# Optimization experiments

Measured on AMD Instinct MI355X. Metric: run time of the kernel, lower is better.

## Reference

```python
import jax, jax.numpy as jnp
import numpy as np

B, C, L, E = 32, 3, 512, 512


def setup_inputs() -> dict:
    key = jax.random.key(0)
    ks = jax.random.split(key, 13)
    bnd = float(np.sqrt(6.0 / (2.0 * E)))  # xavier-uniform-like bound
    uni = lambda k, shp: jax.random.uniform(k, shp, jnp.float32, -bnd, bnd)
    return {
        "A0": jax.random.normal(ks[0], (B, C, L, L), jnp.float32),
        "x0": jax.random.normal(ks[1], (B, C, L, E), jnp.float32),
        "u0": jax.random.normal(ks[2], (B, C, E), jnp.float32),
        "t0": jax.random.normal(ks[3], (B, E), jnp.float32),
        "t1": jax.random.normal(ks[4], (B, E), jnp.float32),
        "Q_weight": uni(ks[5], (C, E, E)),
        "Q_bias": jnp.zeros((C, E), jnp.float32),
        "V_weight": uni(ks[6], (C, E, E)),
        "V_bias": jnp.zeros((C, E), jnp.float32),
        "K_weight": uni(ks[7], (C, E, E)),
        "K_bias": jnp.zeros((C, E), jnp.float32),
        "T_weight": uni(ks[8], (C, E, E)),
        "T_bias": jnp.zeros((C, E), jnp.float32),
    }


def reference(A0, x0, u0, t0, t1,
              Q_weight, Q_bias, V_weight, V_bias,
              K_weight, K_bias, T_weight, T_bias):
    # Time embeddings: (B,E) @ (C,E,E) -> (B,C,E)
    T0 = jnp.einsum('be,cef->bcf', t0, T_weight)
    T1 = jnp.einsum('be,cef->bcf', t1, T_weight)

    # Original modulates weight columns: x @ (W * T) == (x @ W) * T (T broadcasts
    # over the input axis via unsqueeze(-2)); use the fused, equivalent form.
    Q = jnp.einsum('bce,cef->bcf', x0[:, :, -1, :], Q_weight) * T0 + Q_bias  # (B,C,E)
    K = jnp.einsum('bce,cef->bcf', u0, K_weight) * T1 + K_bias               # (B,C,E)
    V = jnp.einsum('bcle,cef->bclf', x0, V_weight) * T1[:, :, None, :] \
        + V_bias[None, :, None, :]                                           # (B,C,L,E)

    QKV = jax.nn.softmax(jnp.einsum('bce,bcle->bcl', Q * K, V), axis=-1)     # (B,C,L)

    # A1[:, :, i, :] = A0[:, :, i+1, :] - A0[:, :, 0, :] for i < L-1;
    # A1[:, :, L-1, :] = A1[:, :, L-2, :] + QKV  (= A0[-1] - A0[0] + QKV)
    rows = A0[:, :, 1:, :] - A0[:, :, :1, :]                                 # (B,C,L-1,L)
    last = rows[:, :, -1, :] + QKV                                           # (B,C,L)
    A1 = jnp.concatenate([rows, last[:, :, None, :]], axis=2)                # (B,C,L,L)

    x1 = jnp.einsum('bclm,bcme->bcle', A1, x0)                               # (B,C,L,E)
    x1 = jnp.diff(x1, axis=2, prepend=jnp.zeros_like(x1[:, :, :1, :]))

    num = jnp.sum(T0 * T1, axis=-1)                                          # (B,C)
    den = jnp.sqrt(jnp.sum(T0 * T0, axis=-1) + jnp.sum(T1 * T1, axis=-1))
    w = (num / den)[..., None]                                               # (B,C,1)

    u1 = u0 * (1.0 - w) + x1.mean(axis=-2) * w                               # (B,C,E)
    return (A1 - A0, x1 - x0, u1 - u0)
```

## Files before the change

kernel.cpp:

```cpp
#include <hip/hip_runtime.h>
#include <stdint.h>

#define BB 32
#define CC 3
#define LL 512
#define EE 512
#define NBC (BB*CC)

#define O2_OFF ((size_t)NBC*LL*LL)
#define O3_OFF (O2_OFF + (size_t)NBC*LL*EE)

#define WSB_QX    0
#define WSB_H     196608
#define WSB_W     442368
#define WSB_ADIFF ((size_t)512*1024)
#define ADIFF_BYTES ((size_t)NBC*LL*LL*2)
#define WSB_X0T   (WSB_ADIFF + ADIFF_BYTES)
#define WS_FAST_NEED (WSB_X0T + ADIFF_BYTES)

#define NEC 16

typedef short bf16x8 __attribute__((ext_vector_type(8)));
typedef float f32x4  __attribute__((ext_vector_type(4)));
typedef unsigned short u16x8 __attribute__((ext_vector_type(8)));

__device__ __forceinline__ float wred_sum(float v){
#pragma unroll
  for (int m = 32; m >= 1; m >>= 1) v += __shfl_xor(v, m, 64);
  return v;
}
__device__ __forceinline__ float wred_max(float v){
#pragma unroll
  for (int m = 32; m >= 1; m >>= 1) v = fmaxf(v, __shfl_xor(v, m, 64));
  return v;
}
__device__ __forceinline__ void f4ma(float4& a, float s, const float4& b){
  a.x = fmaf(s, b.x, a.x); a.y = fmaf(s, b.y, a.y);
  a.z = fmaf(s, b.z, a.z); a.w = fmaf(s, b.w, a.w);
}
__device__ __forceinline__ float4 f4sub(const float4& a, const float4& b){
  return make_float4(a.x-b.x, a.y-b.y, a.z-b.z, a.w-b.w);
}
__device__ __forceinline__ unsigned short f2bf(float x){
  unsigned u = __float_as_uint(x);
  return (unsigned short)((u + 0x7FFFu + ((u >> 16) & 1u)) >> 16);
}
__device__ __forceinline__ float bf2f(unsigned short h){
  return __uint_as_float(((unsigned)h) << 16);
}
__device__ __forceinline__ void split1(float v, unsigned short& hi, unsigned short& lo){
  hi = f2bf(v);
  lo = f2bf(v - bf2f(hi));
}
__device__ __forceinline__ void st_nt_f4(float* p, float4 v){
  f32x4 w; w[0]=v.x; w[1]=v.y; w[2]=v.z; w[3]=v.w;
  __builtin_nontemporal_store(w, reinterpret_cast<f32x4*>(p));
}
__device__ __forceinline__ void st_nt_f(float* p, float v){
  __builtin_nontemporal_store(v, p);
}

__global__ __launch_bounds__(512) void conv2m(
    const float* __restrict__ A0, const float* __restrict__ x0,
    const float* __restrict__ u0,
    const float* __restrict__ t0, const float* __restrict__ t1,
    const float* __restrict__ Qw, const float* __restrict__ Kw,
    const float* __restrict__ Tw,
    char* __restrict__ adiff, char* __restrict__ x0t,
    float* __restrict__ P)
{
  const int bid = blockIdx.x;
  const int t = threadIdx.x;
  __shared__ float T[64][65];
  __shared__ float vb[4][4][32];

  if (bid < 768) {
    const int bc = bid >> 3, tile = bid & 7;
    const int r0 = tile*64;
    const size_t abase = (size_t)bc*LL*LL;
    char* ad = adiff + (size_t)bc*LL*LL*2;
    const int q4 = t & 127, rg = t >> 7;
    const int base = r0 + rg*16;
    float4 prev = *reinterpret_cast<const float4*>(A0 + abase + (size_t)base*LL + q4*4);
#pragma unroll 4
    for (int i = 0; i < 16; ++i) {
      int gr = base + i;
      float4 cur;
      if (gr + 1 < LL)
        cur = *reinterpret_cast<const float4*>(A0 + abase + (size_t)(gr+1)*LL + q4*4);
      else cur = prev;
      float4 d;
      if (gr < LL-1) d = f4sub(cur, prev);
      else           d = make_float4(0.f,0.f,0.f,0.f);
      if ((gr >> 2) == q4) {
        int e = gr & 3;
        d.x -= (e == 0) ? 1.0f : 0.0f;
        d.y -= (e == 1) ? 1.0f : 0.0f;
        d.z -= (e == 2) ? 1.0f : 0.0f;
        d.w -= (e == 3) ? 1.0f : 0.0f;
      }
      ushort4 pk;
      pk.x = f2bf(d.x); pk.y = f2bf(d.y); pk.z = f2bf(d.z); pk.w = f2bf(d.w);
      *reinterpret_cast<ushort4*>(ad + (size_t)gr*1024 + q4*8) = pk;
      prev = cur;
    }
  } else if (bid < 1536) {
    const int bid1 = bid - 768;
    const int bc = bid1 >> 3, tile = bid1 & 7;
    const int m0 = tile*64;
    const size_t xbase = (size_t)bc*LL*EE;
    char* xt = x0t + (size_t)bc*LL*EE*2;
    u16x8 outs[8];
#pragma unroll
    for (int ech = 0; ech < 8; ++ech) {
      const int e0 = ech*64;
      {
        int ml = t >> 3, seg = t & 7;
        const float* src = x0 + xbase + (size_t)(m0+ml)*EE + e0 + seg*8;
        float4 v0 = *reinterpret_cast<const float4*>(src);
        float4 v1 = *reinterpret_cast<const float4*>(src+4);
        T[ml][seg*8+0]=v0.x; T[ml][seg*8+1]=v0.y; T[ml][seg*8+2]=v0.z; T[ml][seg*8+3]=v0.w;
        T[ml][seg*8+4]=v1.x; T[ml][seg*8+5]=v1.y; T[ml][seg*8+6]=v1.z; T[ml][seg*8+7]=v1.w;
      }
      __syncthreads();
      {
        int el = t >> 3, c3 = t & 7;
        int mb = c3*8;
        u16x8 p;
        p[0]=f2bf(T[mb+0][el]); p[1]=f2bf(T[mb+1][el]);
        p[2]=f2bf(T[mb+2][el]); p[3]=f2bf(T[mb+3][el]);
        p[4]=f2bf(T[mb+4][el]); p[5]=f2bf(T[mb+5][el]);
        p[6]=f2bf(T[mb+6][el]); p[7]=f2bf(T[mb+7][el]);
        outs[ech] = p;
      }
      __syncthreads();
    }
    {
      int el = t >> 3, c3 = t & 7;
#pragma unroll
      for (int ech = 0; ech < 8; ++ech) {
        int eg = ech*64 + el;
        *reinterpret_cast<u16x8*>(xt + (size_t)eg*1024 + (size_t)(m0 + c3*8)*2) = outs[ech];
      }
    }
  } else {
    const int idx = bid - 1536;
    const int bg = idx & 7;
    const int rem = idx >> 3;
    const int c  = rem % 3;
    const int ec = rem / 3;
    const int b0 = bg*4;
    const int e0 = ec*32;
    const int f  = t;
    {
      int vec = f >> 7, j = (f >> 5) & 3, e = f & 31;
      int bb = b0 + j;
      float v;
      if      (vec == 0) v = t0[bb*EE + e0 + e];
      else if (vec == 1) v = t1[bb*EE + e0 + e];
      else if (vec == 2) v = x0[((size_t)(bb*CC + c)*LL + (LL-1))*EE + e0 + e];
      else               v = u0[(size_t)(bb*CC + c)*EE + e0 + e];
      vb[vec][j][e] = v;
    }
    __syncthreads();
    const float* twp = Tw + (size_t)c*EE*EE + (size_t)e0*EE + f;
    const float* qwp = Qw + (size_t)c*EE*EE + (size_t)e0*EE + f;
    const float* kwp = Kw + (size_t)c*EE*EE + (size_t)e0*EE + f;
    float aT0[4]={0,0,0,0}, aT1[4]={0,0,0,0}, aQ[4]={0,0,0,0}, aK[4]={0,0,0,0};
#pragma unroll 8
    for (int e = 0; e < 32; ++e) {
      float wt = twp[(size_t)e*EE];
      float wq = qwp[(size_t)e*EE];
      float wk = kwp[(size_t)e*EE];
#pragma unroll
      for (int j = 0; j < 4; ++j) {
        aT0[j] = fmaf(vb[0][j][e], wt, aT0[j]);
        aT1[j] = fmaf(vb[1][j][e], wt, aT1[j]);
        aQ[j]  = fmaf(vb[2][j][e], wq, aQ[j]);
        aK[j]  = fmaf(vb[3][j][e], wk, aK[j]);
      }
    }
#pragma unroll
    for (int j = 0; j < 4; ++j) {
      int cb = c*BB + b0 + j;
      P[(((size_t)0*NEC + ec)*96 + cb)*EE + f] = aT0[j];
      P[(((size_t)1*NEC + ec)*96 + cb)*EE + f] = aT1[j];
      P[(((size_t)2*NEC + ec)*96 + cb)*EE + f] = aQ[j];
      P[(((size_t)3*NEC + ec)*96 + cb)*EE + f] = aK[j];
    }
  }
}

__global__ __launch_bounds__(512) void k0c(
    const float* __restrict__ P,
    const float* __restrict__ Qb, const float* __restrict__ Kb,
    float* __restrict__ gtbuf, float* __restrict__ ws_w)
{
  const int bc = blockIdx.x;
  const int b = bc / CC, c = bc % CC;
  const int cb = c*BB + b;
  const int f = threadIdx.x;
  const int wid = f >> 6, lane = f & 63;
  __shared__ float red[8][3];
  float aT0=0.f, aT1=0.f, aQ=0.f, aK=0.f;
#pragma unroll
  for (int ec = 0; ec < NEC; ++ec) {
    aT0 += P[(((size_t)0*NEC + ec)*96 + cb)*EE + f];
    aT1 += P[(((size_t)1*NEC + ec)*96 + cb)*EE + f];
    aQ  += P[(((size_t)2*NEC + ec)*96 + cb)*EE + f];
    aK  += P[(((size_t)3*NEC + ec)*96 + cb)*EE + f];
  }
  float Qv = aQ*aT0 + Qb[c*EE + f];
  float Kv = aK*aT1 + Kb[c*EE + f];
  gtbuf[(size_t)cb*EE + f] = Qv*Kv*aT1;
  float pn = wred_sum(aT0*aT1);
  float p0 = wred_sum(aT0*aT0);
  float p1 = wred_sum(aT1*aT1);
  if (lane == 0) { red[wid][0]=pn; red[wid][1]=p0; red[wid][2]=p1; }
  __syncthreads();
  if (f == 0) {
    float sn=0.f, s0=0.f, s1=0.f;
    for (int i=0;i<8;++i){ sn+=red[i][0]; s0+=red[i][1]; s1+=red[i][2]; }
    ws_w[bc] = sn / sqrtf(s0 + s1);
  }
}

__global__ __launch_bounds__(256) void k1_h(
    const float* __restrict__ Vw, const float* __restrict__ gtbuf,
    float* __restrict__ ws_h)
{
  const int nt = blockIdx.x;
  const int c  = blockIdx.y;
  const int n0 = nt*128;
  const int t = threadIdx.x, lane = t & 63, w = t >> 6;
  __shared__ __align__(16) char AgtH[32*1024];
  __shared__ __align__(16) char AgtL[32*1024];
  __shared__ __align__(16) char BvH[128*128];
  __shared__ __align__(16) char BvL[128*128];
  {
    int row = t >> 3, sl = t & 7;
    const float* src = gtbuf + ((size_t)(c*BB + row))*EE + sl*64;
#pragma unroll
    for (int c3 = 0; c3 < 8; ++c3) {
      float4 a = *reinterpret_cast<const float4*>(src + c3*8);
      float4 b = *reinterpret_cast<const float4*>(src + c3*8 + 4);
      ushort4 h0,h1,l0,l1;
      split1(a.x,h0.x,l0.x); split1(a.y,h0.y,l0.y); split1(a.z,h0.z,l0.z); split1(a.w,h0.w,l0.w);
      split1(b.x,h1.x,l1.x); split1(b.y,h1.y,l1.y); split1(b.z,h1.z,l1.z); split1(b.w,h1.w,l1.w);
      int off = row*1024 + sl*128 + ((c3 ^ (row & 7)) << 4);
      *reinterpret_cast<ushort4*>(AgtH + off)     = h0;
      *reinterpret_cast<ushort4*>(AgtH + off + 8) = h1;
      *reinterpret_cast<ushort4*>(AgtL + off)     = l0;
      *reinterpret_cast<ushort4*>(AgtL + off + 8) = l1;
    }
  }
  f32x4 acc[2][2];
#pragma unroll
  for (int mi=0; mi<2; ++mi)
#pragma unroll
    for (int ni=0; ni<2; ++ni) acc[mi][ni] = (f32x4){0.f,0.f,0.f,0.f};

  for (int kk = 0; kk < 8; ++kk) {
    __syncthreads();
    {
      int nl = t >> 1, half = t & 1;
      const float* src = Vw + (size_t)c*EE*EE + (size_t)(n0+nl)*EE + kk*64 + half*32;
#pragma unroll
      for (int q = 0; q < 4; ++q) {
        float4 a = *reinterpret_cast<const float4*>(src + q*8);
        float4 b = *reinterpret_cast<const float4*>(src + q*8 + 4);
        int c3 = half*4 + q;
        ushort4 h0,h1,l0,l1;
        split1(a.x,h0.x,l0.x); split1(a.y,h0.y,l0.y); split1(a.z,h0.z,l0.z); split1(a.w,h0.w,l0.w);
        split1(b.x,h1.x,l1.x); split1(b.y,h1.y,l1.y); split1(b.z,h1.z,l1.z); split1(b.w,h1.w,l1.w);
        int off = nl*128 + ((c3 ^ (nl & 7)) << 4);
        *reinterpret_cast<ushort4*>(BvH + off)     = h0;
        *reinterpret_cast<ushort4*>(BvH + off + 8) = h1;
        *reinterpret_cast<ushort4*>(BvL + off)     = l0;
        *reinterpret_cast<ushort4*>(BvL + off + 8) = l1;
      }
    }
    __syncthreads();
    bf16x8 afH[2][2], afL[2][2], bfH[2][2], bfL[2][2];
#pragma unroll
    for (int mi=0; mi<2; ++mi)
#pragma unroll
      for (int ks=0; ks<2; ++ks) {
        int row = mi*16 + (lane & 15);
        int c3 = ks*4 + (lane >> 4);
        int off = row*1024 + kk*128 + ((c3 ^ (row & 7)) << 4);
        afH[mi][ks] = *reinterpret_cast<const bf16x8*>(AgtH + off);
        afL[mi][ks] = *reinterpret_cast<const bf16x8*>(AgtL + off);
      }
#pragma unroll
    for (int ni=0; ni<2; ++ni)
#pragma unroll
      for (int ks=0; ks<2; ++ks) {
        int n = w*32 + ni*16 + (lane & 15);
        int c3 = ks*4 + (lane >> 4);
        int off = n*128 + ((c3 ^ (n & 7)) << 4);
        bfH[ni][ks] = *reinterpret_cast<const bf16x8*>(BvH + off);
        bfL[ni][ks] = *reinterpret_cast<const bf16x8*>(BvL + off);
      }
#pragma unroll
    for (int mi=0; mi<2; ++mi)
#pragma unroll
      for (int ni=0; ni<2; ++ni)
#pragma unroll
        for (int ks=0; ks<2; ++ks) {
          acc[mi][ni] = __builtin_amdgcn_mfma_f32_16x16x32_bf16(afH[mi][ks], bfH[ni][ks], acc[mi][ni], 0, 0, 0);
          acc[mi][ni] = __builtin_amdgcn_mfma_f32_16x16x32_bf16(afH[mi][ks], bfL[ni][ks], acc[mi][ni], 0, 0, 0);
          acc[mi][ni] = __builtin_amdgcn_mfma_f32_16x16x32_bf16(afL[mi][ks], bfH[ni][ks], acc[mi][ni], 0, 0, 0);
        }
  }
#pragma unroll
  for (int mi=0; mi<2; ++mi)
#pragma unroll
    for (int ni=0; ni<2; ++ni)
#pragma unroll
      for (int r=0; r<4; ++r) {
        int b = mi*16 + (lane >> 4)*4 + r;
        int e = n0 + w*32 + ni*16 + (lane & 15);
        ws_h[((size_t)(b*CC + c))*EE + e] = acc[mi][ni][r];
      }
}

__global__ __launch_bounds__(512) void k2f(
    const float* __restrict__ A0, const float* __restrict__ x0,
    const float* __restrict__ u0,
    const float* __restrict__ ws_h, const float* __restrict__ ws_w,
    float* __restrict__ out1, float* __restrict__ out2, float* __restrict__ out3)
{
  const int bc = blockIdx.x;
  const int tid = threadIdx.x, wid = tid >> 6, lane = tid & 63;
  __shared__ __align__(16) float hb[EE], sb[LL], a0r0[LL], a0r3[LL];
  __shared__ float red[8];
  __shared__ float partl[4][12][128];
  const size_t abase = (size_t)bc*LL*LL;
  const size_t xbase = (size_t)bc*LL*EE;
  hb[tid]   = ws_h[(size_t)bc*EE + tid];
  a0r0[tid] = A0[abase + tid];
  a0r3[tid] = A0[abase + (size_t)(LL-1)*LL + tid];
  __syncthreads();
  const float4 h0 = *reinterpret_cast<const float4*>(&hb[lane*8]);
  const float4 h1 = *reinterpret_cast<const float4*>(&hb[lane*8+4]);
  for (int l = wid; l < LL; l += 8) {
    const float4* xr = reinterpret_cast<const float4*>(x0 + xbase + (size_t)l*EE);
    float4 v0 = xr[lane*2], v1 = xr[lane*2+1];
    float acc = v0.x*h0.x + v0.y*h0.y + v0.z*h0.z + v0.w*h0.w
              + v1.x*h1.x + v1.y*h1.y + v1.z*h1.z + v1.w*h1.w;
    acc = wred_sum(acc);
    if (lane == 0) sb[l] = acc;
  }
  __syncthreads();
  float v = sb[tid];
  float mx = wred_max(v);
  if (lane == 0) red[wid] = mx;
  __syncthreads();
  mx = red[0];
#pragma unroll
  for (int i = 1; i < 8; ++i) mx = fmaxf(mx, red[i]);
  float ev = __expf(v - mx);
  float sm = wred_sum(ev);
  __syncthreads();
  if (lane == 0) red[wid] = sm;
  __syncthreads();
  float tot = 0.f;
#pragma unroll
  for (int i = 0; i < 8; ++i) tot += red[i];
  float qk = ev / tot;
  sb[tid] = qk;
  st_nt_f(out1 + abase + (size_t)(LL-1)*LL + tid, qk - a0r0[tid]);
  __syncthreads();
  const int mg = tid >> 7, cg = tid & 127;
  float4 aq = make_float4(0,0,0,0), a0s = make_float4(0,0,0,0), a3s = make_float4(0,0,0,0);
#pragma unroll 4
  for (int i = 0; i < 128; ++i) {
    int m = mg*128 + i;
    float4 xv = *reinterpret_cast<const float4*>(x0 + xbase + (size_t)m*EE + cg*4);
    float qm = sb[m], z0 = a0r0[m], z3 = a0r3[m];
    f4ma(aq, qm, xv); f4ma(a0s, z0, xv); f4ma(a3s, z3, xv);
  }
#pragma unroll
  for (int k = 0; k < 4; ++k) {
    partl[mg][0+k][cg] = (&aq.x)[k];
    partl[mg][4+k][cg] = (&a0s.x)[k];
    partl[mg][8+k][cg] = (&a3s.x)[k];
  }
  __syncthreads();
  if (mg == 0) {
    float wv = ws_w[bc];
    float4 uv  = *reinterpret_cast<const float4*>(u0 + (size_t)bc*EE + cg*4);
    float4 x51 = *reinterpret_cast<const float4*>(x0 + xbase + (size_t)(LL-1)*EE + cg*4);
    float4 qx4, o3;
#pragma unroll
    for (int k = 0; k < 4; ++k) {
      float q = 0.f, y0 = 0.f, y3 = 0.f;
#pragma unroll
      for (int g = 0; g < 4; ++g) {
        q  += partl[g][0+k][cg];
        y0 += partl[g][4+k][cg];
        y3 += partl[g][8+k][cg];
      }
      (&qx4.x)[k] = q;
      (&o3.x)[k] = wv * ((y3 - y0 + q) * (1.f/(float)LL) - (&uv.x)[k]);
    }
    st_nt_f4(out2 + xbase + (size_t)(LL-1)*EE + cg*4, f4sub(qx4, x51));
    st_nt_f4(out3 + (size_t)bc*EE + cg*4, o3);
  }
}

#define ASTR 80
__global__ __launch_bounds__(256) void k3_bf(
    const char* __restrict__ adiff, const char* __restrict__ x0t,
    const float* __restrict__ A0,
    float* __restrict__ out1, float* __restrict__ out2)
{
  const int bc = blockIdx.y;
  const int rt = blockIdx.x >> 2, nt = blockIdx.x & 3;
  const int r0 = rt*128, n0b = nt*128;
  const int t = threadIdx.x;
  const int lane = t & 63, wid = t >> 6;
  const int wr = wid >> 1, wc = wid & 1;
  __shared__ __align__(16) char As[128*ASTR];
  __shared__ __align__(16) char Bs[128*ASTR];
  __shared__ __align__(16) float zr[LL];
  const char* ad = adiff + (size_t)bc*LL*LL*2;
  const char* xt = x0t  + (size_t)bc*LL*EE*2;
  const size_t abase = (size_t)bc*LL*LL;
  const size_t xbase = (size_t)bc*LL*EE;
  zr[t]       = A0[abase + t];
  zr[t + 256] = A0[abase + t + 256];
  f32x4 acc[4][4];
#pragma unroll
  for (int mi=0; mi<4; ++mi)
#pragma unroll
    for (int ni=0; ni<4; ++ni) acc[mi][ni] = (f32x4){0.f,0.f,0.f,0.f};

  for (int k0 = 0; k0 < LL; k0 += 32) {
    __syncthreads();
#pragma unroll
    for (int i = 0; i < 2; ++i) {
      int idx = i*256 + t;
      int row = idx >> 2, c = idx & 3;
      int4 v = *reinterpret_cast<const int4*>(ad + (size_t)(r0+row)*1024 + k0*2 + c*16);
      *reinterpret_cast<int4*>(As + row*ASTR + c*16) = v;
    }
#pragma unroll
    for (int i = 0; i < 2; ++i) {
      int idx = i*256 + t;
      int n = idx >> 2, c = idx & 3;
      int4 v = *reinterpret_cast<const int4*>(xt + (size_t)(n0b+n)*1024 + k0*2 + c*16);
      int kb = (c*16) ^ (((n >> 2) & 3) << 4);
      *reinterpret_cast<int4*>(Bs + n*ASTR + kb) = v;
    }
    __syncthreads();
    bf16x8 af[4], bfv[4];
#pragma unroll
    for (int mi=0; mi<4; ++mi) {
      int row = wr*64 + mi*16 + (lane & 15);
      af[mi] = *reinterpret_cast<const bf16x8*>(As + row*ASTR + ((lane>>4)*16));
    }
#pragma unroll
    for (int ni=0; ni<4; ++ni) {
      int n = wc*64 + ni*16 + (lane & 15);
      int kb = ((lane>>4)*16) ^ (((n >> 2) & 3) << 4);
      bfv[ni] = *reinterpret_cast<const bf16x8*>(Bs + n*ASTR + kb);
    }
#pragma unroll
    for (int mi=0; mi<4; ++mi)
#pragma unroll
      for (int ni=0; ni<4; ++ni)
        acc[mi][ni] = __builtin_amdgcn_mfma_f32_16x16x32_bf16(af[mi], bfv[ni], acc[mi][ni], 0, 0, 0);
    if (((k0 >> 5) & 3) == nt) {
      const int c4 = (t & 7) * 4;
      const int gcol0 = k0 + c4;
      const float4 zz = *reinterpret_cast<const float4*>(&zr[gcol0]);
#pragma unroll
      for (int rr = 0; rr < 4; ++rr) {
        int row = rr*32 + (t >> 3);
        int gr = r0 + row;
        if (gr < LL-1) {
          ushort4 ap = *reinterpret_cast<const ushort4*>(As + row*ASTR + c4*2);
          float4 o;
          o.x = bf2f(ap.x); o.y = bf2f(ap.y); o.z = bf2f(ap.z); o.w = bf2f(ap.w);
          int e = gr - gcol0;
          o.x += (e == 0) ? 1.0f : 0.0f;
          o.y += (e == 1) ? 1.0f : 0.0f;
          o.z += (e == 2) ? 1.0f : 0.0f;
          o.w += (e == 3) ? 1.0f : 0.0f;
          st_nt_f4(out1 + abase + (size_t)gr*LL + gcol0, f4sub(o, zz));
        }
      }
    }
  }
#pragma unroll
  for (int mi=0; mi<4; ++mi)
#pragma unroll
    for (int r=0; r<4; ++r) {
      int grow = r0 + wr*64 + mi*16 + (lane>>4)*4 + r;
      if (grow >= LL-1) continue;
      const size_t rowoff = xbase + (size_t)grow*EE;
#pragma unroll
      for (int ni=0; ni<4; ++ni) {
        int gcol = n0b + wc*64 + ni*16 + (lane & 15);
        st_nt_f(out2 + rowoff + gcol, acc[mi][ni][r]);
      }
    }
}

__global__ __launch_bounds__(512) void kA_fused(
    const float* __restrict__ A0, const float* __restrict__ x0,
    const float* __restrict__ u0,
    const float* __restrict__ t0, const float* __restrict__ t1,
    const float* __restrict__ Qw, const float* __restrict__ Qb,
    const float* __restrict__ Vw,
    const float* __restrict__ Kw, const float* __restrict__ Kb,
    const float* __restrict__ Tw,
    float* __restrict__ ws_qx, float* __restrict__ out1, float* __restrict__ out3)
{
  const int bc = blockIdx.x;
  const int b = bc / CC, c = bc % CC;
  const int tid = threadIdx.x;
  const int wid = tid >> 6, lane = tid & 63;
  __shared__ __align__(16) float t0v[EE], t1v[EE], xl[EE], uv[EE], gt[EE];
  __shared__ __align__(16) float hb[EE], sb[LL], a0r0[LL], a0r3[LL];
  __shared__ float red[3][8];
  __shared__ float wsh;
  const size_t abase = (size_t)bc*LL*LL;
  const size_t xbase = (size_t)bc*LL*EE;

  t0v[tid] = t0[b*EE + tid];
  t1v[tid] = t1[b*EE + tid];
  xl[tid]  = x0[xbase + (size_t)(LL-1)*EE + tid];
  uv[tid]  = u0[(size_t)bc*EE + tid];
  a0r0[tid] = A0[abase + tid];
  a0r3[tid] = A0[abase + (size_t)(LL-1)*LL + tid];
  __syncthreads();

  const int f = tid;
  const float* twp = Tw + (size_t)c*EE*EE + f;
  const float* qwp = Qw + (size_t)c*EE*EE + f;
  const float* kwp = Kw + (size_t)c*EE*EE + f;
  float aT0 = 0.f, aT1 = 0.f, aQ = 0.f, aK = 0.f;
  for (int e = 0; e < EE; ++e) {
    float wt = twp[(size_t)e*EE];
    aT0 = fmaf(t0v[e], wt, aT0);
    aT1 = fmaf(t1v[e], wt, aT1);
    aQ  = fmaf(xl[e],  qwp[(size_t)e*EE], aQ);
    aK  = fmaf(uv[e],  kwp[(size_t)e*EE], aK);
  }
  float Qv = aQ*aT0 + Qb[c*EE + f];
  float Kv = aK*aT1 + Kb[c*EE + f];
  gt[f] = Qv*Kv*aT1;

  float pn = wred_sum(aT0*aT1);
  float p0 = wred_sum(aT0*aT0);
  float p1 = wred_sum(aT1*aT1);
  if (lane == 0) { red[0][wid]=pn; red[1][wid]=p0; red[2][wid]=p1; }
  __syncthreads();
  if (tid == 0) {
    float sn=0.f, s0=0.f, s1=0.f;
    for (int i=0;i<8;++i){ sn+=red[0][i]; s0+=red[1][i]; s1+=red[2][i]; }
    wsh = sn / sqrtf(s0 + s1);
  }
  {
    const float4 g0 = *reinterpret_cast<const float4*>(&gt[lane*8]);
    const float4 g1 = *reinterpret_cast<const float4*>(&gt[lane*8+4]);
    for (int r = wid; r < EE; r += 8) {
      const float4* vr = reinterpret_cast<const float4*>(Vw + ((size_t)c*EE + r)*EE);
      float4 v0 = vr[lane*2], v1 = vr[lane*2+1];
      float acc = v0.x*g0.x + v0.y*g0.y + v0.z*g0.z + v0.w*g0.w
                + v1.x*g1.x + v1.y*g1.y + v1.z*g1.z + v1.w*g1.w;
      acc = wred_sum(acc);
      if (lane == 0) hb[r] = acc;
    }
  }
  __syncthreads();

  {
    const float4 h0 = *reinterpret_cast<const float4*>(&hb[lane*8]);
    const float4 h1 = *reinterpret_cast<const float4*>(&hb[lane*8+4]);
    for (int l = wid; l < LL; l += 8) {
      const float4* xr = reinterpret_cast<const float4*>(x0 + xbase + (size_t)l*EE);
      float4 v0 = xr[lane*2], v1 = xr[lane*2+1];
      float acc = v0.x*h0.x + v0.y*h0.y + v0.z*h0.z + v0.w*h0.w
                + v1.x*h1.x + v1.y*h1.y + v1.z*h1.z + v1.w*h1.w;
      acc = wred_sum(acc);
      if (lane == 0) sb[l] = acc;
    }
  }
  __syncthreads();

  float v = sb[tid];
  float mx = wred_max(v);
  if (lane == 0) red[0][wid] = mx;
  __syncthreads();
  mx = red[0][0];
#pragma unroll
  for (int i = 1; i < 8; ++i) mx = fmaxf(mx, red[0][i]);
  float ev = __expf(v - mx);
  float sm = wred_sum(ev);
  __syncthreads();
  if (lane == 0) red[0][wid] = sm;
  __syncthreads();
  float tot = 0.f;
#pragma unroll
  for (int i = 0; i < 8; ++i) tot += red[0][i];
  float qk = ev / tot;
  sb[tid] = qk;
  out1[abase + (size_t)(LL-1)*LL + tid] = qk - a0r0[tid];
  __syncthreads();

  float qx=0.f, y0=0.f, y3=0.f;
  for (int m = 0; m < LL; ++m) {
    float xm = x0[xbase + (size_t)m*EE + tid];
    qx = fmaf(sb[m],   xm, qx);
    y0 = fmaf(a0r0[m], xm, y0);
    y3 = fmaf(a0r3[m], xm, y3);
  }
  ws_qx[(size_t)bc*EE + tid] = qx;
  float mean = (y3 - y0 + qx) * (1.f/(float)LL);
  out3[(size_t)bc*EE + tid] = wsh * (mean - uv[tid]);
}

__global__ __launch_bounds__(256) void k3_mfma(
    const float* __restrict__ A0, const float* __restrict__ x0,
    const float* __restrict__ ws_qx,
    float* __restrict__ out1, float* __restrict__ out2)
{
  const int bc = blockIdx.y;
  const int rt = blockIdx.x >> 2, nt = blockIdx.x & 3;
  const int r0 = rt*128, n0b = nt*128;
  const int t = threadIdx.x;
  const int lane = t & 63, wid = t >> 6;
  const int wr = wid >> 1, wc = wid & 1;
  __shared__ __align__(16) char As[128*ASTR];
  __shared__ __align__(16) char Bs[128*ASTR];
  const size_t abase = (size_t)bc*LL*LL;
  const size_t xbase = (size_t)bc*LL*EE;
  f32x4 acc[4][4];
#pragma unroll
  for (int mi=0; mi<4; ++mi)
#pragma unroll
    for (int ni=0; ni<4; ++ni) acc[mi][ni] = (f32x4){0.f,0.f,0.f,0.f};
  const int bkl = (t & 7) * 4;
  const int bn0 = (t >> 3) * 4;
  for (int k0 = 0; k0 < LL; k0 += 32) {
    __syncthreads();
#pragma unroll
    for (int i = 0; i < 4; ++i) {
      int idx = i*256 + t;
      int row = idx >> 3, kq = idx & 7;
      int gr = r0 + row;
      int gr1 = (gr+1 > LL-1) ? (LL-1) : (gr+1);
      float4 va = *reinterpret_cast<const float4*>(A0 + abase + (size_t)gr *LL + k0 + kq*4);
      float4 vb = *reinterpret_cast<const float4*>(A0 + abase + (size_t)gr1*LL + k0 + kq*4);
      ushort4 pk;
      pk.x = f2bf(vb.x - va.x); pk.y = f2bf(vb.y - va.y);
      pk.z = f2bf(vb.z - va.z); pk.w = f2bf(vb.w - va.w);
      *reinterpret_cast<ushort4*>(As + row*ASTR + kq*8) = pk;
      if (nt == 0 && gr < LL-1) {
        float4 az = *reinterpret_cast<const float4*>(A0 + abase + k0 + kq*4);
        float4 o = make_float4(vb.x - az.x - va.x, vb.y - az.y - va.y,
                               vb.z - az.z - va.z, vb.w - az.w - va.w);
        *reinterpret_cast<float4*>(out1 + abase + (size_t)gr*LL + k0 + kq*4) = o;
      }
    }
    {
      float xq[4][4];
#pragma unroll
      for (int i = 0; i < 4; ++i)
        *reinterpret_cast<float4*>(xq[i]) =
          *reinterpret_cast<const float4*>(x0 + xbase + (size_t)(k0+bkl+i)*EE + n0b + bn0);
#pragma unroll
      for (int j = 0; j < 4; ++j) {
        int n = bn0 + j;
        ushort4 pk;
        pk.x = f2bf(xq[0][j]); pk.y = f2bf(xq[1][j]);
        pk.z = f2bf(xq[2][j]); pk.w = f2bf(xq[3][j]);
        int kb = (bkl*2) ^ (((n >> 2) & 3) << 4);
        *reinterpret_cast<ushort4*>(Bs + n*ASTR + kb) = pk;
      }
    }
    __syncthreads();
    bf16x8 af[4], bfv[4];
#pragma unroll
    for (int mi=0; mi<4; ++mi) {
      int row = wr*64 + mi*16 + (lane & 15);
      af[mi] = *reinterpret_cast<const bf16x8*>(As + row*ASTR + ((lane>>4)*16));
    }
#pragma unroll
    for (int ni=0; ni<4; ++ni) {
      int n = wc*64 + ni*16 + (lane & 15);
      int kb = ((lane>>4)*16) ^ (((n >> 2) & 3) << 4);
      bfv[ni] = *reinterpret_cast<const bf16x8*>(Bs + n*ASTR + kb);
    }
#pragma unroll
    for (int mi=0; mi<4; ++mi)
#pragma unroll
      for (int ni=0; ni<4; ++ni)
        acc[mi][ni] = __builtin_amdgcn_mfma_f32_16x16x32_bf16(af[mi], bfv[ni], acc[mi][ni], 0, 0, 0);
  }
#pragma unroll
  for (int mi=0; mi<4; ++mi)
#pragma unroll
    for (int r=0; r<4; ++r) {
      int grow = r0 + wr*64 + mi*16 + (lane>>4)*4 + r;
      const size_t rowoff = xbase + (size_t)grow*EE;
#pragma unroll
      for (int ni=0; ni<4; ++ni) {
        int gcol = n0b + wc*64 + ni*16 + (lane & 15);
        float xv = x0[rowoff + gcol];
        float val;
        if (grow == LL-1) val = ws_qx[(size_t)bc*EE + gcol] - xv;
        else              val = acc[mi][ni][r] - xv;
        out2[rowoff + gcol] = val;
      }
    }
}

extern "C" void kernel_launch(void* const* d_in, const int* in_sizes, int n_in,
                              void* d_out, int out_size, void* d_ws, size_t ws_size,
                              hipStream_t stream)
{
  const float* A0 = (const float*)d_in[0];
  const float* x0 = (const float*)d_in[1];
  const float* u0 = (const float*)d_in[2];
  const float* t0 = (const float*)d_in[3];
  const float* t1 = (const float*)d_in[4];
  const float* Qw = (const float*)d_in[5];
  const float* Qb = (const float*)d_in[6];
  const float* Vw = (const float*)d_in[7];
  const float* Kw = (const float*)d_in[9];
  const float* Kb = (const float*)d_in[10];
  const float* Tw = (const float*)d_in[11];

  char*  wsb    = (char*)d_ws;
  float* ws_qx  = (float*)(wsb + WSB_QX);
  float* ws_h   = (float*)(wsb + WSB_H);
  float* ws_w   = (float*)(wsb + WSB_W);

  float* out1 = (float*)d_out;
  float* out2 = out1 + O2_OFF;
  float* out3 = out1 + O3_OFF;
  float* gtbuf = out3;
  float* pscr  = out2;

  const bool fast = ws_size >= WS_FAST_NEED;

  if (fast) {
    char* adiff = wsb + WSB_ADIFF;
    char* x0t   = wsb + WSB_X0T;
    conv2m<<<1920, 512, 0, stream>>>(A0, x0, u0, t0, t1, Qw, Kw, Tw,
                                     adiff, x0t, pscr);
    k0c<<<NBC, 512, 0, stream>>>(pscr, Qb, Kb, gtbuf, ws_w);
    k1_h<<<dim3(4, 3), 256, 0, stream>>>(Vw, gtbuf, ws_h);
    k2f<<<NBC, 512, 0, stream>>>(A0, x0, u0, ws_h, ws_w, out1, out2, out3);
    k3_bf<<<dim3(16, NBC), 256, 0, stream>>>(adiff, x0t, A0, out1, out2);
  } else {
    kA_fused<<<NBC, 512, 0, stream>>>(A0, x0, u0, t0, t1, Qw, Qb, Vw, Kw, Kb, Tw,
                                      ws_qx, out1, out3);
    k3_mfma<<<dim3(16, NBC), 256, 0, stream>>>(A0, x0, ws_qx, out1, out2);
  }
}
```

Before: 233.4 us.

## Fuse x0 transpose and bf16 conversion into GEMM B-tile load

Removes the separate pre-pass in conv2m that transposed x0 into a bf16 buffer, and instead has k3_bf load fp32 x0 tiles directly, convert them to bf16 and store them transposed into shared memory. This drops a full write and re-read of a bf16 copy of x0 (about 50MB of round-trip traffic) and shrinks the conv2m grid. In exchange, k3_bf now reads fp32 x0 (twice the bytes per B tile) once per row tile, four times per batch-channel, and does the conversion and scattered 8-byte LDS stores inside the main loop.

```diff
diff --git a/kernel.cpp b/kernel.cpp
--- a/kernel.cpp
+++ b/kernel.cpp
@@ -15,8 +15,7 @@
 #define WSB_W     442368
 #define WSB_ADIFF ((size_t)512*1024)
 #define ADIFF_BYTES ((size_t)NBC*LL*LL*2)
-#define WSB_X0T   (WSB_ADIFF + ADIFF_BYTES)
-#define WS_FAST_NEED (WSB_X0T + ADIFF_BYTES)
+#define WS_FAST_NEED (WSB_ADIFF + ADIFF_BYTES)
 
 #define NEC 16
 
@@ -66,12 +65,11 @@
     const float* __restrict__ t0, const float* __restrict__ t1,
     const float* __restrict__ Qw, const float* __restrict__ Kw,
     const float* __restrict__ Tw,
-    char* __restrict__ adiff, char* __restrict__ x0t,
+    char* __restrict__ adiff,
     float* __restrict__ P)
 {
   const int bid = blockIdx.x;
   const int t = threadIdx.x;
-  __shared__ float T[64][65];
   __shared__ float vb[4][4][32];
 
   if (bid < 768) {
@@ -104,47 +102,8 @@
       *reinterpret_cast<ushort4*>(ad + (size_t)gr*1024 + q4*8) = pk;
       prev = cur;
     }
-  } else if (bid < 1536) {
-    const int bid1 = bid - 768;
-    const int bc = bid1 >> 3, tile = bid1 & 7;
-    const int m0 = tile*64;
-    const size_t xbase = (size_t)bc*LL*EE;
-    char* xt = x0t + (size_t)bc*LL*EE*2;
-    u16x8 outs[8];
-#pragma unroll
-    for (int ech = 0; ech < 8; ++ech) {
-      const int e0 = ech*64;
-      {
-        int ml = t >> 3, seg = t & 7;
-        const float* src = x0 + xbase + (size_t)(m0+ml)*EE + e0 + seg*8;
-        float4 v0 = *reinterpret_cast<const float4*>(src);
-        float4 v1 = *reinterpret_cast<const float4*>(src+4);
-        T[ml][seg*8+0]=v0.x; T[ml][seg*8+1]=v0.y; T[ml][seg*8+2]=v0.z; T[ml][seg*8+3]=v0.w;
-        T[ml][seg*8+4]=v1.x; T[ml][seg*8+5]=v1.y; T[ml][seg*8+6]=v1.z; T[ml][seg*8+7]=v1.w;
-      }
-      __syncthreads();
-      {
-        int el = t >> 3, c3 = t & 7;
-        int mb = c3*8;
-        u16x8 p;
-        p[0]=f2bf(T[mb+0][el]); p[1]=f2bf(T[mb+1][el]);
-        p[2]=f2bf(T[mb+2][el]); p[3]=f2bf(T[mb+3][el]);
-        p[4]=f2bf(T[mb+4][el]); p[5]=f2bf(T[mb+5][el]);
-        p[6]=f2bf(T[mb+6][el]); p[7]=f2bf(T[mb+7][el]);
-        outs[ech] = p;
-      }
-      __syncthreads();
-    }
-    {
-      int el = t >> 3, c3 = t & 7;
-#pragma unroll
-      for (int ech = 0; ech < 8; ++ech) {
-        int eg = ech*64 + el;
-        *reinterpret_cast<u16x8*>(xt + (size_t)eg*1024 + (size_t)(m0 + c3*8)*2) = outs[ech];
-      }
-    }
   } else {
-    const int idx = bid - 1536;
+    const int idx = bid - 768;
     const int bg = idx & 7;
     const int rem = idx >> 3;
     const int c  = rem % 3;
@@ -412,7 +371,7 @@
 
 #define ASTR 80
 __global__ __launch_bounds__(256) void k3_bf(
-    const char* __restrict__ adiff, const char* __restrict__ x0t,
+    const char* __restrict__ adiff, const float* __restrict__ x0,
     const float* __restrict__ A0,
     float* __restrict__ out1, float* __restrict__ out2)
 {
@@ -426,7 +385,6 @@
   __shared__ __align__(16) char Bs[128*ASTR];
   __shared__ __align__(16) float zr[LL];
   const char* ad = adiff + (size_t)bc*LL*LL*2;
-  const char* xt = x0t  + (size_t)bc*LL*EE*2;
   const size_t abase = (size_t)bc*LL*LL;
   const size_t xbase = (size_t)bc*LL*EE;
   zr[t]       = A0[abase + t];
@@ -437,6 +395,9 @@
 #pragma unroll
     for (int ni=0; ni<4; ++ni) acc[mi][ni] = (f32x4){0.f,0.f,0.f,0.f};
 
+  const int bkl = (t & 7) * 4;
+  const int bn0 = (t >> 3) * 4;
+
   for (int k0 = 0; k0 < LL; k0 += 32) {
     __syncthreads();
 #pragma unroll
@@ -446,13 +407,21 @@
       int4 v = *reinterpret_cast<const int4*>(ad + (size_t)(r0+row)*1024 + k0*2 + c*16);
       *reinterpret_cast<int4*>(As + row*ASTR + c*16) = v;
     }
-#pragma unroll
-    for (int i = 0; i < 2; ++i) {
-      int idx = i*256 + t;
-      int n = idx >> 2, c = idx & 3;
-      int4 v = *reinterpret_cast<const int4*>(xt + (size_t)(n0b+n)*1024 + k0*2 + c*16);
-      int kb = (c*16) ^ (((n >> 2) & 3) << 4);
-      *reinterpret_cast<int4*>(Bs + n*ASTR + kb) = v;
+    {
+      float xq[4][4];
+#pragma unroll
+      for (int i = 0; i < 4; ++i)
+        *reinterpret_cast<float4*>(xq[i]) =
+          *reinterpret_cast<const float4*>(x0 + xbase + (size_t)(k0+bkl+i)*EE + n0b + bn0);
+#pragma unroll
+      for (int j = 0; j < 4; ++j) {
+        int n = bn0 + j;
+        ushort4 pk;
+        pk.x = f2bf(xq[0][j]); pk.y = f2bf(xq[1][j]);
+        pk.z = f2bf(xq[2][j]); pk.w = f2bf(xq[3][j]);
+        int kb = (bkl*2) ^ (((n >> 2) & 3) << 4);
+        *reinterpret_cast<ushort4*>(Bs + n*ASTR + kb) = pk;
+      }
     }
     __syncthreads();
     bf16x8 af[4], bfv[4];
@@ -751,13 +720,12 @@
 
   if (fast) {
     char* adiff = wsb + WSB_ADIFF;
-    char* x0t   = wsb + WSB_X0T;
-    conv2m<<<1920, 512, 0, stream>>>(A0, x0, u0, t0, t1, Qw, Kw, Tw,
-                                     adiff, x0t, pscr);
+    conv2m<<<1152, 512, 0, stream>>>(A0, x0, u0, t0, t1, Qw, Kw, Tw,
+                                     adiff, pscr);
     k0c<<<NBC, 512, 0, stream>>>(pscr, Qb, Kb, gtbuf, ws_w);
     k1_h<<<dim3(4, 3), 256, 0, stream>>>(Vw, gtbuf, ws_h);
     k2f<<<NBC, 512, 0, stream>>>(A0, x0, u0, ws_h, ws_w, out1, out2, out3);
-    k3_bf<<<dim3(16, NBC), 256, 0, stream>>>(adiff, x0t, A0, out1, out2);
+    k3_bf<<<dim3(16, NBC), 256, 0, stream>>>(adiff, x0, A0, out1, out2);
   } else {
     kA_fused<<<NBC, 512, 0, stream>>>(A0, x0, u0, t0, t1, Qw, Qb, Vw, Kw, Kb, Tw,
                                       ws_qx, out1, out3);
```

Measured after the change: 230.8 us. Within noise of the previous version (-1.1%).
